# Optimization experiments

Measured on AMD Instinct MI355X. Metric: run time of the kernel, lower is better.

## Reference

```python
import jax, jax.numpy as jnp
import numpy as np

HEADS = 16
EPS = 1e-6


def setup_inputs() -> dict:
    key = jax.random.key(0)
    k1, k2, k3 = jax.random.split(key, 3)
    B, N, C = 4, 4096, 1024
    x = jax.random.normal(k1, (B, N, C), dtype=jnp.float32)
    w_qkv = jax.random.normal(k2, (3 * C, C), dtype=jnp.float32) * (C ** -0.5)
    w_out = jax.random.normal(k3, (C, C), dtype=jnp.float32) * (C ** -0.5)
    b_out = jnp.zeros((C,), dtype=jnp.float32)
    return {"x": x, "w_qkv": w_qkv, "w_out": w_out, "b_out": b_out}


def reference(x, w_qkv, w_out, b_out):
    B, N, C = x.shape
    H = HEADS
    D = C // H
    scale = D ** -0.25

    qkv = x @ w_qkv.T  # [B, N, 3C]
    q, k, v = jnp.split(qkv, 3, axis=-1)

    def heads(t):  # [B, N, C] -> [B, H, N, D]
        return t.reshape(B, N, H, D).transpose(0, 2, 1, 3)

    q, k, v = heads(q), heads(k), heads(v)

    feat = lambda t: jax.nn.elu(t) + 1.0
    q = feat(q) * scale
    k = feat(k) * scale

    kv = jnp.einsum('bhnd,bhne->bhde', k, v)      # [B, H, D, D]
    out = jnp.einsum('bhnd,bhde->bhne', q, kv)    # [B, H, N, D]
    k_sum = k.sum(axis=2)                          # [B, H, D]
    denom = jnp.einsum('bhnd,bhd->bhn', q, k_sum)  # [B, H, N]
    out = out / (denom[..., None] + EPS)

    out = out.transpose(0, 2, 1, 3).reshape(B, N, C)
    return out @ w_out.T + b_out
```

## Files before the change

### kernel.cpp

```cpp
#include <hip/hip_runtime.h>
#include <hip/hip_bf16.h>
#include <cmath>


typedef __bf16 bf16_t;
typedef __attribute__((ext_vector_type(8))) __bf16 bf16x8;
typedef __attribute__((ext_vector_type(4))) __bf16 bf16x4;
typedef __attribute__((ext_vector_type(4))) float f32x4;
typedef __attribute__((ext_vector_type(8))) float f32x8;

#define MFMA16(a, b, c) __builtin_amdgcn_mfma_f32_16x16x32_bf16((a), (b), (c), 0, 0, 0)

#define LDS_PITCH 72

__device__ __forceinline__ f32x4 zf4() { f32x4 z; z[0] = 0.f; z[1] = 0.f; z[2] = 0.f; z[3] = 0.f; return z; }

__device__ __forceinline__ float feat(float x) { return x > 0.f ? x + 1.f : expf(x); }

__device__ __forceinline__ void gld_lds16(const bf16_t* src, bf16_t* dst)
{
    __builtin_amdgcn_global_load_lds(
        (__attribute__((address_space(1))) void*)const_cast<bf16_t*>(src),
        (__attribute__((address_space(3))) void*)dst, 16, 0, 0);
}

template <int NR>
__device__ __forceinline__ void stage_async(const bf16_t* g, int ld, bf16_t* lds, int tid)
{
    const int w = tid >> 6, l = tid & 63;
    constexpr int CALLS = NR >> 5;
#pragma unroll
    for (int p = 0; p < CALLS; ++p) {
        const int chunk = w * CALLS + p;
        const int gidx = chunk * 64 + l;
        const int row = gidx >> 3;
        const int cp = gidx & 7;
        const int c = cp ^ (row & 7);
        gld_lds16(g + row * ld + c * 8, lds + chunk * 512);
    }
}

__device__ __forceinline__ bf16x8 read_frag_sw(const bf16_t* lds, int row, int cg)
{
    const int sw = cg ^ (row & 7);
    return *(const bf16x8*)(lds + row * 64 + sw * 8);
}

template <int NR>
__device__ __forceinline__ void stage_bf16(const bf16_t* g, int ld, bf16_t* lds, int tid)
{
#pragma unroll
    for (int p = 0; p < NR * 8 / 256; ++p) {
        const int gidx = p * 256 + tid;
        const int row = gidx >> 3;
        const int cp = gidx & 7;
        *(bf16x8*)(lds + row * LDS_PITCH + cp * 8) = *(const bf16x8*)(g + row * ld + cp * 8);
    }
}

__device__ __forceinline__ bf16x8 read_frag(const bf16_t* lds, int row, int cg)
{
    return *(const bf16x8*)(lds + row * LDS_PITCH + cg * 8);
}

__global__ __launch_bounds__(256) void cvt_kernel(const float* __restrict__ src, bf16_t* __restrict__ dst)
{
    const size_t idx = ((size_t)blockIdx.x * 256 + threadIdx.x) * 8;
    f32x8 f = *(const f32x8*)(src + idx);
    bf16x8 v;
#pragma unroll
    for (int t = 0; t < 8; ++t) v[t] = (bf16_t)f[t];
    *(bf16x8*)(dst + idx) = v;
}

template <int MODE>
__global__ __launch_bounds__(256, 3) void gemm_bt_kernel(
    const bf16_t* __restrict__ A, const bf16_t* __restrict__ B, int K,
    void* __restrict__ out0, bf16_t* __restrict__ out1, bf16_t* __restrict__ out2,
    const float* __restrict__ bias)
{
    __shared__ __align__(16) bf16_t As[128 * 64];
    __shared__ __align__(16) bf16_t Bs[128 * 64];
    const int tid = threadIdx.x;
    const int l = tid & 63, w = tid >> 6;
    const int wm = w >> 1, wn = w & 1;
    const int quad = l >> 4, r16 = l & 15;
    const int m0 = blockIdx.y * 128;
    const int n0 = blockIdx.x * 128;

    f32x4 acc[4][4];
#pragma unroll
    for (int i = 0; i < 4; ++i)
#pragma unroll
        for (int j = 0; j < 4; ++j) acc[i][j] = zf4();

    const bf16_t* Ab = A + (size_t)m0 * K;
    const bf16_t* Bb = B + (size_t)n0 * K;

    for (int k0 = 0; k0 < K; k0 += 64) {
        stage_async<128>(Ab + k0, K, As, tid);
        stage_async<128>(Bb + k0, K, Bs, tid);
        __syncthreads();
#pragma unroll
        for (int ks = 0; ks < 2; ++ks) {
            const int cg = ks * 4 + quad;
            bf16x8 af[4], bfr[4];
#pragma unroll
            for (int i = 0; i < 4; ++i) af[i] = read_frag_sw(As, wm * 64 + i * 16 + r16, cg);
#pragma unroll
            for (int j = 0; j < 4; ++j) bfr[j] = read_frag_sw(Bs, wn * 64 + j * 16 + r16, cg);
#pragma unroll
            for (int i = 0; i < 4; ++i)
#pragma unroll
                for (int j = 0; j < 4; ++j)
                    acc[i][j] = MFMA16(af[i], bfr[j], acc[i][j]);
        }
        __syncthreads();
    }

    const float scale = 0.3535533905932738f;
#pragma unroll
    for (int i = 0; i < 4; ++i) {
        const int mbase = m0 + wm * 64 + i * 16 + quad * 4;
#pragma unroll
        for (int j = 0; j < 4; ++j) {
            const int col = n0 + wn * 64 + j * 16 + r16;
            if (MODE == 1) {
                float* yp = (float*)out0;
                const float bb = bias[col];
#pragma unroll
                for (int r = 0; r < 4; ++r)
                    yp[(size_t)(mbase + r) * 1024 + col] = acc[i][j][r] + bb;
            } else {
                const int part = col >> 10;
                const int cc = col & 1023;
                const int hh = (mbase >> 12) * 16 + (cc >> 6);
                const int d = cc & 63;
                const int ntok = mbase & 4095;
                if (part == 0) {
                    bf16_t* qp = (bf16_t*)out0 + ((size_t)hh * 4096 + ntok) * 64 + d;
#pragma unroll
                    for (int r = 0; r < 4; ++r)
                        qp[(size_t)r * 64] = (bf16_t)(feat(acc[i][j][r]) * scale);
                } else {
                    bf16_t* tp = (part == 1 ? out1 : out2) + ((size_t)hh * 64 + d) * 4096 + ntok;
                    bf16x4 pk;
#pragma unroll
                    for (int r = 0; r < 4; ++r) {
                        float v = acc[i][j][r];
                        if (part == 1) v = feat(v) * scale;
                        pk[r] = (bf16_t)v;
                    }
                    *(bf16x4*)tp = pk;
                }
            }
        }
    }
}

__global__ __launch_bounds__(256, 2) void kv_partial_kernel(
    const bf16_t* __restrict__ KT, const bf16_t* __restrict__ VT,
    float* __restrict__ kvp, float* __restrict__ ksp_out)
{
    __shared__ __align__(16) bf16_t Ks[64 * LDS_PITCH];
    __shared__ __align__(16) bf16_t Vs[64 * LDS_PITCH];
    const int tid = threadIdx.x;
    const int l = tid & 63, w = tid >> 6;
    const int quad = l >> 4, r16 = l & 15;
    const int hh = blockIdx.x;
    const int ksp = blockIdx.y;
    const bf16_t* kb = KT + (size_t)hh * 64 * 4096 + ksp * 1024;
    const bf16_t* vb = VT + (size_t)hh * 64 * 4096 + ksp * 1024;

    bf16x8 ones;
#pragma unroll
    for (int t = 0; t < 8; ++t) ones[t] = (bf16_t)1.0f;

    f32x4 acc[4], accks[4];
#pragma unroll
    for (int j = 0; j < 4; ++j) { acc[j] = zf4(); accks[j] = zf4(); }

    for (int k0 = 0; k0 < 1024; k0 += 64) {
        stage_bf16<64>(kb + k0, 4096, Ks, tid);
        stage_bf16<64>(vb + k0, 4096, Vs, tid);
        __syncthreads();
#pragma unroll
        for (int ks = 0; ks < 2; ++ks) {
            const int cg = ks * 4 + quad;
            bf16x8 af = read_frag(Vs, w * 16 + r16, cg);
            bf16x8 bk[4];
#pragma unroll
            for (int j = 0; j < 4; ++j) bk[j] = read_frag(Ks, j * 16 + r16, cg);
#pragma unroll
            for (int j = 0; j < 4; ++j) acc[j] = MFMA16(af, bk[j], acc[j]);
            if (w == 0) {
#pragma unroll
                for (int j = 0; j < 4; ++j) accks[j] = MFMA16(ones, bk[j], accks[j]);
            }
        }
        __syncthreads();
    }

    float* ob = kvp + (size_t)(hh * 4 + ksp) * 4096;
    const int ebase = w * 16 + quad * 4;
#pragma unroll
    for (int j = 0; j < 4; ++j)
#pragma unroll
        for (int r = 0; r < 4; ++r)
            ob[(ebase + r) * 64 + j * 16 + r16] = acc[j][r];

    if (w == 0 && quad == 0) {
        float* kso = ksp_out + (size_t)(hh * 4 + ksp) * 64;
#pragma unroll
        for (int j = 0; j < 4; ++j) kso[j * 16 + r16] = accks[j][0];
    }
}

__global__ __launch_bounds__(256) void kvfix_kernel(
    const float* __restrict__ kvp, const float* __restrict__ ksp,
    bf16_t* __restrict__ kvb, bf16_t* __restrict__ ksumb)
{
    const int hh = blockIdx.x, t = threadIdx.x;
    const float* base = kvp + (size_t)hh * 4 * 4096;
    const int off = t * 16;
    bf16x8 o[2];
#pragma unroll
    for (int c = 0; c < 4; ++c) {
        f32x4 s = *(const f32x4*)(base + off + c * 4);
        s += *(const f32x4*)(base + 4096 + off + c * 4);
        s += *(const f32x4*)(base + 8192 + off + c * 4);
        s += *(const f32x4*)(base + 12288 + off + c * 4);
#pragma unroll
        for (int r = 0; r < 4; ++r) o[c >> 1][(c & 1) * 4 + r] = (bf16_t)s[r];
    }
    *(bf16x8*)(kvb + (size_t)hh * 4096 + off) = o[0];
    *(bf16x8*)(kvb + (size_t)hh * 4096 + off + 8) = o[1];
    if (t < 64) {
        const float* kb = ksp + (size_t)hh * 4 * 64;
        ksumb[(size_t)hh * 64 + t] = (bf16_t)(kb[t] + kb[64 + t] + kb[128 + t] + kb[192 + t]);
    }
}

__global__ __launch_bounds__(256, 2) void attn_out_kernel(
    const bf16_t* __restrict__ Q, const bf16_t* __restrict__ kvb, const bf16_t* __restrict__ ksumb,
    bf16_t* __restrict__ att)
{
    __shared__ __align__(16) bf16_t kvT[64 * LDS_PITCH];
    __shared__ __align__(16) bf16_t ksb[64];
    const int tid = threadIdx.x;
    const int l = tid & 63, w = tid >> 6;
    const int quad = l >> 4, r16 = l & 15;
    const int hh = blockIdx.x;
    const int b = hh >> 4, h = hh & 15;
    const int mt = blockIdx.y;

    {
        const int e = tid >> 2, d0 = (tid & 3) * 16;
        const bf16_t* kvbh = kvb + (size_t)hh * 4096;
        *(bf16x8*)(kvT + e * LDS_PITCH + d0)     = *(const bf16x8*)(kvbh + e * 64 + d0);
        *(bf16x8*)(kvT + e * LDS_PITCH + d0 + 8) = *(const bf16x8*)(kvbh + e * 64 + d0 + 8);
        if (tid < 64) ksb[tid] = ksumb[(size_t)hh * 64 + tid];
    }
    __syncthreads();

    f32x4 acc[4][4];
    f32x4 dacc[4];
#pragma unroll
    for (int i = 0; i < 4; ++i) {
        dacc[i] = zf4();
#pragma unroll
        for (int j = 0; j < 4; ++j) acc[i][j] = zf4();
    }

    const int m0w = mt * 256 + w * 64;
    const bf16_t* qb = Q + (size_t)hh * 4096 * 64;
#pragma unroll
    for (int ks = 0; ks < 2; ++ks) {
        bf16x8 kf = *(const bf16x8*)(ksb + ks * 32 + quad * 8);
        if (r16 != 0) {
#pragma unroll
            for (int t = 0; t < 8; ++t) kf[t] = (bf16_t)0.f;
        }
        bf16x8 bfr[4];
#pragma unroll
        for (int j = 0; j < 4; ++j)
            bfr[j] = *(const bf16x8*)(kvT + (j * 16 + r16) * LDS_PITCH + ks * 32 + quad * 8);
#pragma unroll
        for (int i = 0; i < 4; ++i) {
            const bf16_t* qp = qb + (size_t)(m0w + i * 16 + r16) * 64 + ks * 32 + quad * 8;
            const bf16x8 af = *(const bf16x8*)qp;
            dacc[i] = MFMA16(af, kf, dacc[i]);
#pragma unroll
            for (int j = 0; j < 4; ++j) acc[i][j] = MFMA16(af, bfr[j], acc[i][j]);
        }
    }

#pragma unroll
    for (int i = 0; i < 4; ++i) {
        float den[4];
#pragma unroll
        for (int r = 0; r < 4; ++r)
            den[r] = __shfl(dacc[i][r], l & 48) + 1e-6f;
#pragma unroll
        for (int j = 0; j < 4; ++j) {
            const size_t colb = (size_t)h * 64 + j * 16 + r16;
#pragma unroll
            for (int r = 0; r < 4; ++r) {
                const int ntok = m0w + i * 16 + quad * 4 + r;
                att[((size_t)b * 4096 + ntok) * 1024 + colb] = (bf16_t)(acc[i][j][r] / den[r]);
            }
        }
    }
}

extern "C" void kernel_launch(void* const* d_in, const int* in_sizes, int n_in,
                              void* d_out, int out_size, void* d_ws, size_t ws_size,
                              hipStream_t stream)
{
    const float* x    = (const float*)d_in[0];
    const float* wqkv = (const float*)d_in[1];
    const float* wout = (const float*)d_in[2];
    const float* bout = (const float*)d_in[3];
    float* y = (float*)d_out;

    char* ws = (char*)d_ws;
    bf16_t* xb    = (bf16_t*)ws;
    bf16_t* wqkvb = (bf16_t*)(ws + (size_t)32 * 1048576);
    bf16_t* woutb = (bf16_t*)(ws + (size_t)38 * 1048576);
    bf16_t* Q     = (bf16_t*)(ws + (size_t)40 * 1048576);
    bf16_t* KT    = (bf16_t*)(ws + (size_t)72 * 1048576);
    bf16_t* VT    = (bf16_t*)(ws + (size_t)104 * 1048576);
    float* kvp    = (float*)ws;
    float* ksp    = (float*)(ws + (size_t)4 * 1048576);
    bf16_t* kvb   = (bf16_t*)(ws + (size_t)5 * 1048576);
    bf16_t* ksumb = (bf16_t*)(ws + (size_t)6 * 1048576);
    bf16_t* att   = KT;

    cvt_kernel<<<8192, 256, 0, stream>>>(x, xb);
    cvt_kernel<<<1536, 256, 0, stream>>>(wqkv, wqkvb);
    cvt_kernel<<<512, 256, 0, stream>>>(wout, woutb);

    gemm_bt_kernel<0><<<dim3(24, 128), 256, 0, stream>>>(xb, wqkvb, 1024, Q, KT, VT, nullptr);
    kv_partial_kernel<<<dim3(64, 4), 256, 0, stream>>>(KT, VT, kvp, ksp);
    kvfix_kernel<<<64, 256, 0, stream>>>(kvp, ksp, kvb, ksumb);
    attn_out_kernel<<<dim3(64, 16), 256, 0, stream>>>(Q, kvb, ksumb, att);
    gemm_bt_kernel<1><<<dim3(8, 128), 256, 0, stream>>>(att, woutb, 1024, y, nullptr, nullptr, bout);
}
```

Baseline: 326.7 us.

## Use 32x32 MFMA in GEMMs, fuse conversions, load KV fragments directly

```diff
diff --git a/kernel.cpp b/kernel.cpp
--- a/kernel.cpp
+++ b/kernel.cpp
@@ -8,8 +8,10 @@
 typedef __attribute__((ext_vector_type(4))) __bf16 bf16x4;
 typedef __attribute__((ext_vector_type(4))) float f32x4;
 typedef __attribute__((ext_vector_type(8))) float f32x8;
+typedef __attribute__((ext_vector_type(16))) float f32x16;
 
 #define MFMA16(a, b, c) __builtin_amdgcn_mfma_f32_16x16x32_bf16((a), (b), (c), 0, 0, 0)
+#define MFMA32(a, b, c) __builtin_amdgcn_mfma_f32_32x32x16_bf16((a), (b), (c), 0, 0, 0)
 
 #define LDS_PITCH 72
 
@@ -46,31 +48,23 @@
     return *(const bf16x8*)(lds + row * 64 + sw * 8);
 }
 
-template <int NR>
-__device__ __forceinline__ void stage_bf16(const bf16_t* g, int ld, bf16_t* lds, int tid)
-{
-#pragma unroll
-    for (int p = 0; p < NR * 8 / 256; ++p) {
-        const int gidx = p * 256 + tid;
-        const int row = gidx >> 3;
-        const int cp = gidx & 7;
-        *(bf16x8*)(lds + row * LDS_PITCH + cp * 8) = *(const bf16x8*)(g + row * ld + cp * 8);
-    }
-}
-
-__device__ __forceinline__ bf16x8 read_frag(const bf16_t* lds, int row, int cg)
-{
-    return *(const bf16x8*)(lds + row * LDS_PITCH + cg * 8);
-}
-
-__global__ __launch_bounds__(256) void cvt_kernel(const float* __restrict__ src, bf16_t* __restrict__ dst)
-{
-    const size_t idx = ((size_t)blockIdx.x * 256 + threadIdx.x) * 8;
-    f32x8 f = *(const f32x8*)(src + idx);
+__global__ __launch_bounds__(256) void cvt_all_kernel(
+    const float* __restrict__ x, bf16_t* __restrict__ xb,
+    const float* __restrict__ wqkv, bf16_t* __restrict__ wqkvb,
+    const float* __restrict__ wout, bf16_t* __restrict__ woutb)
+{
+    const int g = blockIdx.x * 256 + threadIdx.x;
+    const float* src;
+    bf16_t* dst;
+    size_t off;
+    if (g < 2097152)      { src = x;    dst = xb;    off = (size_t)g * 8; }
+    else if (g < 2490368) { src = wqkv; dst = wqkvb; off = (size_t)(g - 2097152) * 8; }
+    else                  { src = wout; dst = woutb; off = (size_t)(g - 2490368) * 8; }
+    f32x8 f = *(const f32x8*)(src + off);
     bf16x8 v;
 #pragma unroll
     for (int t = 0; t < 8; ++t) v[t] = (bf16_t)f[t];
-    *(bf16x8*)(dst + idx) = v;
+    *(bf16x8*)(dst + off) = v;
 }
 
 template <int MODE>
@@ -84,15 +78,17 @@
     const int tid = threadIdx.x;
     const int l = tid & 63, w = tid >> 6;
     const int wm = w >> 1, wn = w & 1;
-    const int quad = l >> 4, r16 = l & 15;
+    const int lid = l & 31, half = l >> 5;
     const int m0 = blockIdx.y * 128;
     const int n0 = blockIdx.x * 128;
 
-    f32x4 acc[4][4];
-#pragma unroll
-    for (int i = 0; i < 4; ++i)
-#pragma unroll
-        for (int j = 0; j < 4; ++j) acc[i][j] = zf4();
+    f32x16 acc[2][2];
+#pragma unroll
+    for (int i = 0; i < 2; ++i)
+#pragma unroll
+        for (int j = 0; j < 2; ++j)
+#pragma unroll
+            for (int r = 0; r < 16; ++r) acc[i][j][r] = 0.f;
 
     const bf16_t* Ab = A + (size_t)m0 * K;
     const bf16_t* Bb = B + (size_t)n0 * K;
@@ -102,68 +98,73 @@
         stage_async<128>(Bb + k0, K, Bs, tid);
         __syncthreads();
 #pragma unroll
-        for (int ks = 0; ks < 2; ++ks) {
-            const int cg = ks * 4 + quad;
-            bf16x8 af[4], bfr[4];
-#pragma unroll
-            for (int i = 0; i < 4; ++i) af[i] = read_frag_sw(As, wm * 64 + i * 16 + r16, cg);
-#pragma unroll
-            for (int j = 0; j < 4; ++j) bfr[j] = read_frag_sw(Bs, wn * 64 + j * 16 + r16, cg);
-#pragma unroll
-            for (int i = 0; i < 4; ++i)
-#pragma unroll
-                for (int j = 0; j < 4; ++j)
-                    acc[i][j] = MFMA16(af[i], bfr[j], acc[i][j]);
+        for (int s = 0; s < 4; ++s) {
+            const int cg = s * 2 + half;
+            bf16x8 af[2], bfr[2];
+#pragma unroll
+            for (int i = 0; i < 2; ++i) af[i] = read_frag_sw(As, wm * 64 + i * 32 + lid, cg);
+#pragma unroll
+            for (int j = 0; j < 2; ++j) bfr[j] = read_frag_sw(Bs, wn * 64 + j * 32 + lid, cg);
+#pragma unroll
+            for (int i = 0; i < 2; ++i)
+#pragma unroll
+                for (int j = 0; j < 2; ++j)
+                    acc[i][j] = MFMA32(af[i], bfr[j], acc[i][j]);
         }
         __syncthreads();
     }
 
     const float scale = 0.3535533905932738f;
 #pragma unroll
-    for (int i = 0; i < 4; ++i) {
-        const int mbase = m0 + wm * 64 + i * 16 + quad * 4;
-#pragma unroll
-        for (int j = 0; j < 4; ++j) {
-            const int col = n0 + wn * 64 + j * 16 + r16;
+    for (int i = 0; i < 2; ++i) {
+        const int rowb = m0 + wm * 64 + i * 32 + 4 * half;
+#pragma unroll
+        for (int j = 0; j < 2; ++j) {
+            const int col = n0 + wn * 64 + j * 32 + lid;
             if (MODE == 1) {
                 float* yp = (float*)out0;
                 const float bb = bias[col];
 #pragma unroll
-                for (int r = 0; r < 4; ++r)
-                    yp[(size_t)(mbase + r) * 1024 + col] = acc[i][j][r] + bb;
+                for (int r = 0; r < 16; ++r) {
+                    const int row = rowb + (r & 3) + 8 * (r >> 2);
+                    yp[(size_t)row * 1024 + col] = acc[i][j][r] + bb;
+                }
             } else {
                 const int part = col >> 10;
                 const int cc = col & 1023;
-                const int hh = (mbase >> 12) * 16 + (cc >> 6);
+                const int hh = (rowb >> 12) * 16 + (cc >> 6);
                 const int d = cc & 63;
-                const int ntok = mbase & 4095;
                 if (part == 0) {
-                    bf16_t* qp = (bf16_t*)out0 + ((size_t)hh * 4096 + ntok) * 64 + d;
-#pragma unroll
-                    for (int r = 0; r < 4; ++r)
-                        qp[(size_t)r * 64] = (bf16_t)(feat(acc[i][j][r]) * scale);
+                    bf16_t* qp = (bf16_t*)out0 + ((size_t)hh * 4096) * 64 + d;
+#pragma unroll
+                    for (int r = 0; r < 16; ++r) {
+                        const int ntok = (rowb + (r & 3) + 8 * (r >> 2)) & 4095;
+                        qp[(size_t)ntok * 64] = (bf16_t)(feat(acc[i][j][r]) * scale);
+                    }
                 } else {
-                    bf16_t* tp = (part == 1 ? out1 : out2) + ((size_t)hh * 64 + d) * 4096 + ntok;
-                    bf16x4 pk;
-#pragma unroll
-                    for (int r = 0; r < 4; ++r) {
-                        float v = acc[i][j][r];
-                        if (part == 1) v = feat(v) * scale;
-                        pk[r] = (bf16_t)v;
+                    bf16_t* tp = (part == 1 ? out1 : out2) + ((size_t)hh * 64 + d) * 4096;
+#pragma unroll
+                    for (int rg = 0; rg < 4; ++rg) {
+                        const int ntok = (rowb + 8 * rg) & 4095;
+                        bf16x4 pk;
+#pragma unroll
+                        for (int r = 0; r < 4; ++r) {
+                            float v = acc[i][j][rg * 4 + r];
+                            if (part == 1) v = feat(v) * scale;
+                            pk[r] = (bf16_t)v;
+                        }
+                        *(bf16x4*)(tp + ntok) = pk;
                     }
-                    *(bf16x4*)tp = pk;
                 }
             }
         }
     }
 }
 
-__global__ __launch_bounds__(256, 2) void kv_partial_kernel(
+__global__ __launch_bounds__(256) void kv_partial_kernel(
     const bf16_t* __restrict__ KT, const bf16_t* __restrict__ VT,
     float* __restrict__ kvp, float* __restrict__ ksp_out)
 {
-    __shared__ __align__(16) bf16_t Ks[64 * LDS_PITCH];
-    __shared__ __align__(16) bf16_t Vs[64 * LDS_PITCH];
     const int tid = threadIdx.x;
     const int l = tid & 63, w = tid >> 6;
     const int quad = l >> 4, r16 = l & 15;
@@ -180,25 +181,20 @@
 #pragma unroll
     for (int j = 0; j < 4; ++j) { acc[j] = zf4(); accks[j] = zf4(); }
 
-    for (int k0 = 0; k0 < 1024; k0 += 64) {
-        stage_bf16<64>(kb + k0, 4096, Ks, tid);
-        stage_bf16<64>(vb + k0, 4096, Vs, tid);
-        __syncthreads();
-#pragma unroll
-        for (int ks = 0; ks < 2; ++ks) {
-            const int cg = ks * 4 + quad;
-            bf16x8 af = read_frag(Vs, w * 16 + r16, cg);
-            bf16x8 bk[4];
-#pragma unroll
-            for (int j = 0; j < 4; ++j) bk[j] = read_frag(Ks, j * 16 + r16, cg);
-#pragma unroll
-            for (int j = 0; j < 4; ++j) acc[j] = MFMA16(af, bk[j], acc[j]);
-            if (w == 0) {
-#pragma unroll
-                for (int j = 0; j < 4; ++j) accks[j] = MFMA16(ones, bk[j], accks[j]);
-            }
-        }
-        __syncthreads();
+#pragma unroll 4
+    for (int kc = 0; kc < 32; ++kc) {
+        const int koff = kc * 32 + quad * 8;
+        const bf16x8 af = *(const bf16x8*)(vb + (size_t)(w * 16 + r16) * 4096 + koff);
+        bf16x8 bk[4];
+#pragma unroll
+        for (int j = 0; j < 4; ++j)
+            bk[j] = *(const bf16x8*)(kb + (size_t)(j * 16 + r16) * 4096 + koff);
+#pragma unroll
+        for (int j = 0; j < 4; ++j) acc[j] = MFMA16(af, bk[j], acc[j]);
+        if (w == 0) {
+#pragma unroll
+            for (int j = 0; j < 4; ++j) accks[j] = MFMA16(ones, bk[j], accks[j]);
+        }
     }
 
     float* ob = kvp + (size_t)(hh * 4 + ksp) * 4096;
@@ -336,9 +332,7 @@
     bf16_t* ksumb = (bf16_t*)(ws + (size_t)6 * 1048576);
     bf16_t* att   = KT;
 
-    cvt_kernel<<<8192, 256, 0, stream>>>(x, xb);
-    cvt_kernel<<<1536, 256, 0, stream>>>(wqkv, wqkvb);
-    cvt_kernel<<<512, 256, 0, stream>>>(wout, woutb);
+    cvt_all_kernel<<<10240, 256, 0, stream>>>(x, xb, wqkv, wqkvb, wout, woutb);
 
     gemm_bt_kernel<0><<<dim3(24, 128), 256, 0, stream>>>(xb, wqkvb, 1024, Q, KT, VT, nullptr);
     kv_partial_kernel<<<dim3(64, 4), 256, 0, stream>>>(KT, VT, kvp, ksp);
```

After: 345.5 us. 1.06x slower.
